# Kernel optimization log

Measured on AMD Instinct MI355X. Metric: run time of the kernel, lower is better.

Reference implementation:

```python
import jax, jax.numpy as jnp
import numpy as np

N_AUTHOR, N_FOS, N_INST, N_PAPER = 100000, 30000, 8000, 200000
D_IN, D_OUT = 128, 128
# (name, n_src, n_dst, n_edges)
RELS = [("aff", N_AUTHOR, N_INST, 150000), ("ita", N_INST, N_AUTHOR, 150000),
        ("writes", N_AUTHOR, N_PAPER, 500000), ("pta", N_PAPER, N_AUTHOR, 500000),
        ("cites", N_PAPER, N_PAPER, 1000000), ("topic", N_PAPER, N_FOS, 500000),
        ("ftp", N_FOS, N_PAPER, 500000)]
NODE_SIZES = {"author": N_AUTHOR, "fos": N_FOS, "inst": N_INST, "paper": N_PAPER}


def setup_inputs() -> dict:
    key = jax.random.key(0)
    ks = iter(jax.random.split(key, 64))
    inp = {}
    for nt, n in NODE_SIZES.items():
        inp[f"x_{nt}"] = jax.random.normal(next(ks), (n, D_IN), jnp.float32)
    for name, ns, nd, e in RELS:
        inp[f"src_{name}"] = jax.random.randint(next(ks), (e,), 0, ns, jnp.int64)
        inp[f"dst_{name}"] = jax.random.randint(next(ks), (e,), 0, nd, jnp.int64)
    w_scale = 1.0 / np.sqrt(D_IN)
    for nt in NODE_SIZES:
        inp[f"W_root_{nt}"] = jax.random.uniform(next(ks), (D_IN, D_OUT), jnp.float32, -w_scale, w_scale)
        inp[f"b_root_{nt}"] = jax.random.uniform(next(ks), (D_OUT,), jnp.float32, -w_scale, w_scale)
    for name, _, _, _ in RELS:
        inp[f"W_{name}"] = jax.random.uniform(next(ks), (D_IN, D_OUT), jnp.float32, -w_scale, w_scale)
    return inp


def _mean_agg(x_src, src, dst, n_dst):
    # gather source features along edges, mean-reduce into destinations
    msg = x_src[src]                                             # [E, D_IN]
    s = jax.ops.segment_sum(msg, dst, num_segments=n_dst)        # [n_dst, D_IN]
    cnt = jax.ops.segment_sum(jnp.ones_like(dst, dtype=x_src.dtype), dst, num_segments=n_dst)
    return s / jnp.maximum(cnt, 1.0)[:, None]                    # isolated nodes -> 0


def reference(x_author, x_fos, x_inst, x_paper,
              W_root_author, b_root_author, W_root_fos, b_root_fos,
              W_root_inst, b_root_inst, W_root_paper, b_root_paper,
              W_aff, W_ita, W_writes, W_pta, W_cites, W_topic, W_ftp,
              src_aff, dst_aff, src_ita, dst_ita, src_writes, dst_writes,
              src_pta, dst_pta, src_cites, dst_cites, src_topic, dst_topic,
              src_ftp, dst_ftp):
    # root (self) transforms
    out_author = x_author @ W_root_author + b_root_author
    out_fos = x_fos @ W_root_fos + b_root_fos
    out_inst = x_inst @ W_root_inst + b_root_inst
    out_paper = x_paper @ W_root_paper + b_root_paper
    # per-relation aggregate -> linear -> accumulate into destination type
    out_inst = out_inst + _mean_agg(x_author, src_aff, dst_aff, N_INST) @ W_aff
    out_author = out_author + _mean_agg(x_inst, src_ita, dst_ita, N_AUTHOR) @ W_ita
    out_paper = out_paper + _mean_agg(x_author, src_writes, dst_writes, N_PAPER) @ W_writes
    out_author = out_author + _mean_agg(x_paper, src_pta, dst_pta, N_AUTHOR) @ W_pta
    out_paper = out_paper + _mean_agg(x_paper, src_cites, dst_cites, N_PAPER) @ W_cites
    out_fos = out_fos + _mean_agg(x_paper, src_topic, dst_topic, N_FOS) @ W_topic
    out_paper = out_paper + _mean_agg(x_fos, src_ftp, dst_ftp, N_PAPER) @ W_ftp
    # concatenate per-type outputs (author, fos, inst, paper) along node axis
    return jnp.concatenate([out_author, out_fos, out_inst, out_paper], axis=0)
```

## Files before the change

### kernel.cpp

```cpp
#include <hip/hip_runtime.h>

#define N_AUTHOR 100000
#define N_FOS    30000
#define N_INST   8000
#define N_PAPER  200000
#define NCNT     838000
#define ETOT     3300000
#define NSHARD   (NCNT / 8)

#define NBA 1563
#define NBF 469
#define NBI 125
#define NBP 3125
#define NB_TOTAL (NBP + NBA + NBF + NBI)

#define B_AFF    0
#define B_ITA    8000
#define B_WRITES 108000
#define B_PTA    308000
#define B_CITES  408000
#define B_TOPIC  608000
#define B_FTP    638000

typedef __attribute__((ext_vector_type(8))) short short8v;
typedef __attribute__((ext_vector_type(4))) float float4v;
typedef unsigned short us;

__device__ __forceinline__ us f2bf(float f) {
  unsigned u = __float_as_uint(f);
  u = u + 0x7fffu + ((u >> 16) & 1u);
  return (us)(u >> 16);
}
#define BF2F(s) __uint_as_float(((unsigned)(us)(s)) << 16)

__device__ __forceinline__ void acc8(float4v& x, float4v& y, short8v h) {
  x[0] += BF2F(h[0]); x[1] += BF2F(h[1]); x[2] += BF2F(h[2]); x[3] += BF2F(h[3]);
  y[0] += BF2F(h[4]); y[1] += BF2F(h[5]); y[2] += BF2F(h[6]); y[3] += BF2F(h[7]);
}

__device__ __forceinline__ short8v pack8(float4v a, float4v b) {
  short8v h;
  h[0] = (short)f2bf(a[0]); h[1] = (short)f2bf(a[1]);
  h[2] = (short)f2bf(a[2]); h[3] = (short)f2bf(a[3]);
  h[4] = (short)f2bf(b[0]); h[5] = (short)f2bf(b[1]);
  h[6] = (short)f2bf(b[2]); h[7] = (short)f2bf(b[3]);
  return h;
}

#define O_CNT    0
#define O_OFFS   3352000
#define O_CURSOR 6704000
#define O_BTOT   10056000
#define O_CSR    10060096
#define O_WT     23260096
#define XB_AUTHOR 23620544
#define XB_FOS    49220544
#define XB_INST   56900544
#define XB_PAPER  58948544
#define WS_NEED_BF 110148544ULL

struct RelTab { const int* src; const int* dst; int E; int base; };
struct Rels { RelTab r[7]; };
struct WPtrs { const float* w[11]; };
struct XCvt { const float* x; us* xb; int n8; };

__global__ __launch_bounds__(256, 8) void prep(WPtrs P, us* __restrict__ wt,
                     int* __restrict__ cnt,
                     XCvt x0, XCvt x1, XCvt x2, XCvt x3,
                     Rels R, int doX) {
  int gsz = gridDim.x * blockDim.x;
  int gtid = blockIdx.x * blockDim.x + threadIdx.x;
  for (int i = gtid; i < 11 * 16384; i += gsz) {
    int mat = i >> 14, rem = i & 16383;
    int k = rem >> 7, n = rem & 127;
    wt[mat * 16384 + n * 128 + k] = f2bf(P.w[mat][rem]);
  }
  if (doX) {
    XCvt xc[4] = {x0, x1, x2, x3};
    #pragma unroll
    for (int a = 0; a < 4; ++a) {
      const float* xp = xc[a].x;
      short8v* xbp = (short8v*)xc[a].xb;
      int n8 = xc[a].n8;
      for (int i = gtid; i < n8; i += gsz) {
        float4v v0 = *(const float4v*)(xp + (size_t)i * 8);
        float4v v1 = *(const float4v*)(xp + (size_t)i * 8 + 4);
        xbp[i] = pack8(v0, v1);
      }
    }
  }
  const int cls = blockIdx.x & 7;
  const int lo = cls * NSHARD;
  const int hi = lo + NSHARD;
  const int sgsz = (gridDim.x >> 3) * 256;
  const int sgtid = (blockIdx.x >> 3) * 256 + threadIdx.x;
  #pragma unroll
  for (int rr = 0; rr < 7; ++rr) {
    const int* __restrict__ dst = R.r[rr].dst;
    const int E = R.r[rr].E, base = R.r[rr].base;
    for (int e = sgtid; e < E; e += sgsz) {
      int gd = base + dst[e];
      if (gd >= lo && gd < hi) atomicAdd(&cnt[gd], 1);
    }
  }
}

__global__ void scan1(const int* __restrict__ cnt, int* __restrict__ offs,
                      int* __restrict__ btot, int n) {
  __shared__ int sh[256];
  int tid = threadIdx.x;
  int base = blockIdx.x * 2048 + tid * 8;
  int v[8]; int s = 0;
  #pragma unroll
  for (int i = 0; i < 8; ++i) { v[i] = (base + i < n) ? cnt[base + i] : 0; s += v[i]; }
  sh[tid] = s; __syncthreads();
  for (int off = 1; off < 256; off <<= 1) {
    int t = (tid >= off) ? sh[tid - off] : 0;
    __syncthreads();
    sh[tid] += t;
    __syncthreads();
  }
  int excl = sh[tid] - s;
  if (tid == 255) btot[blockIdx.x] = sh[255];
  int run = excl;
  #pragma unroll
  for (int i = 0; i < 8; ++i) { if (base + i < n) offs[base + i] = run; run += v[i]; }
}

__global__ void scan23(int* __restrict__ offs, int* __restrict__ cursor,
                       const int* __restrict__ btot, int nb, int n) {
  __shared__ int sh[512];
  int tid = threadIdx.x;
  int v = (tid < nb) ? btot[tid] : 0;
  sh[tid] = v; __syncthreads();
  for (int off = 1; off < 512; off <<= 1) {
    int t = (tid >= off) ? sh[tid - off] : 0;
    __syncthreads();
    sh[tid] += t;
    __syncthreads();
  }
  int excl = sh[tid] - v;
  __syncthreads();
  sh[tid] = excl;
  __syncthreads();
  int gsz = gridDim.x * 512;
  for (int idx = blockIdx.x * 512 + tid; idx < n; idx += gsz) {
    int val = offs[idx] + sh[idx >> 11];
    offs[idx] = val;
    cursor[idx] = val;
  }
}

__global__ __launch_bounds__(256, 8) void fill_sh(Rels R, int* __restrict__ cursor,
                                                  int* __restrict__ csr) {
  const int cls = blockIdx.x & 7;
  const int lo = cls * NSHARD;
  const int hi = lo + NSHARD;
  const int gsz = (gridDim.x >> 3) * 256;
  const int gtid = (blockIdx.x >> 3) * 256 + threadIdx.x;
  #pragma unroll
  for (int rr = 0; rr < 7; ++rr) {
    const int* __restrict__ src = R.r[rr].src;
    const int* __restrict__ dst = R.r[rr].dst;
    const int E = R.r[rr].E, base = R.r[rr].base;
    for (int e = gtid; e < E; e += gsz) {
      int gd = base + dst[e];
      if (gd >= lo && gd < hi) {
        int p = atomicAdd(&cursor[gd], 1);
        csr[p] = src[e];
      }
    }
  }
}

template <int NSRC>
__device__ __forceinline__ void fused_body(
    const us* __restrict__ x0, const us* __restrict__ x1,
    const us* __restrict__ x2, const us* __restrict__ x3,
    const us* __restrict__ w0, const us* __restrict__ w1,
    const us* __restrict__ w2, const us* __restrict__ w3,
    int b1, int b2, int b3,
    const int* __restrict__ offs, const int* __restrict__ cnt,
    const int* __restrict__ csr,
    const float* __restrict__ bias, float* __restrict__ out, int n, int rb0) {
  const int lane = threadIdx.x & 63;
  const int wv = threadIdx.x >> 6;
  const int rb = rb0 + wv * 16;
  int ar = rb + (lane & 15); if (ar >= n) ar = n - 1;
  const int cw = (lane >> 4) * 8;

  const us* xs[4] = {x0, x1, x2, x3};
  const us* wsp[4] = {w0, w1, w2, w3};
  const int bases[4] = {0, b1, b2, b3};

  int stA[4], dgA[4];
  #pragma unroll
  for (int kb = 1; kb < NSRC; ++kb) {
    int gd = bases[kb] + ar;
    stA[kb] = offs[gd];
    dgA[kb] = cnt[gd];
  }

  float4v acc[8];
  #pragma unroll
  for (int i = 0; i < 8; ++i) acc[i] = (float4v)0.0f;

  #pragma unroll
  for (int kb = 0; kb < NSRC; ++kb) {
    short8v af[4];
    if (kb == 0) {
      const us* rp = xs[0] + (size_t)ar * 128 + cw;
      #pragma unroll
      for (int ks = 0; ks < 4; ++ks)
        af[ks] = *(const short8v*)(rp + ks * 32);
    } else {
      const int st = stA[kb], deg = dgA[kb];
      const us* xb = xs[kb];
      float4v a0[4], a1[4];
      #pragma unroll
      for (int ks = 0; ks < 4; ++ks) { a0[ks] = (float4v)0.f; a1[ks] = (float4v)0.f; }
      int j = 0;
      int s0 = 0, s1 = 0;
      if (deg >= 2) { s0 = csr[st]; s1 = csr[st + 1]; }
      for (; j + 2 <= deg; j += 2) {
        const us* p0 = xb + (size_t)s0 * 128 + cw;
        const us* p1 = xb + (size_t)s1 * 128 + cw;
        if (j + 4 <= deg) { s0 = csr[st + j + 2]; s1 = csr[st + j + 3]; }
        #pragma unroll
        for (int ks = 0; ks < 4; ++ks) {
          short8v h0 = *(const short8v*)(p0 + ks * 32);
          short8v h1 = *(const short8v*)(p1 + ks * 32);
          acc8(a0[ks], a1[ks], h0);
          acc8(a0[ks], a1[ks], h1);
        }
      }
      if (j < deg) {
        int sl = csr[st + j];
        const us* p0 = xb + (size_t)sl * 128 + cw;
        #pragma unroll
        for (int ks = 0; ks < 4; ++ks) {
          short8v h0 = *(const short8v*)(p0 + ks * 32);
          acc8(a0[ks], a1[ks], h0);
        }
      }
      float sc = 1.0f / (float)((deg > 0) ? deg : 1);
      #pragma unroll
      for (int ks = 0; ks < 4; ++ks)
        af[ks] = pack8(a0[ks] * sc, a1[ks] * sc);
    }
    const us* wb = wsp[kb] + (size_t)(lane & 15) * 128 + cw;
    #pragma unroll
    for (int ct = 0; ct < 8; ++ct) {
      short8v bfr[4];
      #pragma unroll
      for (int ks = 0; ks < 4; ++ks)
        bfr[ks] = *(const short8v*)(wb + ct * 2048 + ks * 32);
      #pragma unroll
      for (int ks = 0; ks < 4; ++ks)
        acc[ct] = __builtin_amdgcn_mfma_f32_16x16x32_bf16(af[ks], bfr[ks], acc[ct], 0, 0, 0);
    }
  }
  #pragma unroll
  for (int ct = 0; ct < 8; ++ct) {
    #pragma unroll
    for (int i = 0; i < 4; ++i) {
      int g = rb + (lane >> 4) * 4 + i;
      if (g < n) {
        int col = ct * 16 + (lane & 15);
        out[(size_t)g * 128 + col] = acc[ct][i] + bias[col];
      }
    }
  }
}

__global__ __launch_bounds__(256, 6) void fused_all(
    const us* __restrict__ xbA, const us* __restrict__ xbF,
    const us* __restrict__ xbI, const us* __restrict__ xbP,
    const us* __restrict__ wt,
    const int* __restrict__ offs, const int* __restrict__ cnt,
    const int* __restrict__ csr,
    const float* __restrict__ bA, const float* __restrict__ bF,
    const float* __restrict__ bI, const float* __restrict__ bP,
    float* __restrict__ out) {
  const int bid = blockIdx.x;
  if (bid < NBP) {
    fused_body<4>(xbP, xbA, xbP, xbF,
                  wt + 3 * 16384, wt + 6 * 16384, wt + 8 * 16384, wt + 10 * 16384,
                  B_WRITES, B_CITES, B_FTP, offs, cnt, csr,
                  bP, out + (size_t)138000 * 128, N_PAPER, bid * 64);
  } else if (bid < NBP + NBA) {
    fused_body<3>(xbA, xbI, xbP, nullptr,
                  wt + 0 * 16384, wt + 5 * 16384, wt + 7 * 16384, nullptr,
                  B_ITA, B_PTA, 0, offs, cnt, csr,
                  bA, out, N_AUTHOR, (bid - NBP) * 64);
  } else if (bid < NBP + NBA + NBF) {
    fused_body<2>(xbF, xbP, nullptr, nullptr,
                  wt + 1 * 16384, wt + 9 * 16384, nullptr, nullptr,
                  B_TOPIC, 0, 0, offs, cnt, csr,
                  bF, out + (size_t)100000 * 128, N_FOS, (bid - NBP - NBA) * 64);
  } else {
    fused_body<2>(xbI, xbA, nullptr, nullptr,
                  wt + 2 * 16384, wt + 4 * 16384, nullptr, nullptr,
                  B_AFF, 0, 0, offs, cnt, csr,
                  bI, out + (size_t)130000 * 128, N_INST, (bid - NBP - NBA - NBF) * 64);
  }
}

typedef float4v f4;
__global__ __launch_bounds__(256, 4) void fb_gemm(
    const float* __restrict__ x0, const float* __restrict__ x1,
    const float* __restrict__ x2, const float* __restrict__ x3,
    const us* __restrict__ w0, const us* __restrict__ w1,
    const us* __restrict__ w2, const us* __restrict__ w3,
    int nsrc, int b1, int b2, int b3,
    const int* __restrict__ offs, const int* __restrict__ cnt,
    const int* __restrict__ csr,
    const float* __restrict__ bias, float* __restrict__ out, int n) {
  const int lane = threadIdx.x & 63;
  const int wv = threadIdx.x >> 6;
  const int rb = blockIdx.x * 64 + wv * 16;
  int ar = rb + (lane & 15); if (ar >= n) ar = n - 1;
  const int cw = (lane >> 4) * 8;
  const float* xs[4] = {x0, x1, x2, x3};
  const us* wsp[4] = {w0, w1, w2, w3};
  const int bases[4] = {0, b1, b2, b3};
  float4v acc[8];
  #pragma unroll
  for (int i = 0; i < 8; ++i) acc[i] = (float4v)0.0f;
  for (int kb = 0; kb < nsrc; ++kb) {
    short8v af[4];
    const float* xb = xs[kb];
    if (kb == 0) {
      const float* rp = xb + (size_t)ar * 128 + cw;
      #pragma unroll
      for (int ks = 0; ks < 4; ++ks) {
        f4 u = *(const f4*)(rp + ks * 32);
        f4 v = *(const f4*)(rp + ks * 32 + 4);
        af[ks] = pack8(u, v);
      }
    } else {
      int gd = bases[kb] + ar;
      int st = offs[gd];
      int deg = cnt[gd];
      f4 a0[4], a1[4];
      #pragma unroll
      for (int ks = 0; ks < 4; ++ks) { a0[ks] = (f4)0.f; a1[ks] = (f4)0.f; }
      for (int j = 0; j < deg; ++j) {
        int s0 = csr[st + j];
        const float* p0 = xb + (size_t)s0 * 128 + cw;
        #pragma unroll
        for (int ks = 0; ks < 4; ++ks) {
          a0[ks] += *(const f4*)(p0 + ks * 32);
          a1[ks] += *(const f4*)(p0 + ks * 32 + 4);
        }
      }
      float sc = 1.0f / (float)((deg > 0) ? deg : 1);
      #pragma unroll
      for (int ks = 0; ks < 4; ++ks)
        af[ks] = pack8(a0[ks] * sc, a1[ks] * sc);
    }
    const us* wb = wsp[kb] + (size_t)(lane & 15) * 128 + cw;
    #pragma unroll
    for (int ct = 0; ct < 8; ++ct) {
      short8v bfr[4];
      #pragma unroll
      for (int ks = 0; ks < 4; ++ks)
        bfr[ks] = *(const short8v*)(wb + ct * 2048 + ks * 32);
      #pragma unroll
      for (int ks = 0; ks < 4; ++ks)
        acc[ct] = __builtin_amdgcn_mfma_f32_16x16x32_bf16(af[ks], bfr[ks], acc[ct], 0, 0, 0);
    }
  }
  #pragma unroll
  for (int ct = 0; ct < 8; ++ct) {
    #pragma unroll
    for (int i = 0; i < 4; ++i) {
      int g = rb + (lane >> 4) * 4 + i;
      if (g < n) {
        int col = ct * 16 + (lane & 15);
        out[(size_t)g * 128 + col] = acc[ct][i] + bias[col];
      }
    }
  }
}

extern "C" void kernel_launch(void* const* d_in, const int* in_sizes, int n_in,
                              void* d_out, int out_size, void* d_ws, size_t ws_size,
                              hipStream_t stream) {
  const float* x_author = (const float*)d_in[0];
  const float* x_fos    = (const float*)d_in[1];
  const float* x_inst   = (const float*)d_in[2];
  const float* x_paper  = (const float*)d_in[3];

  Rels R;
  const int E[7]  = {150000, 150000, 500000, 500000, 1000000, 500000, 500000};
  const int ND[7] = {N_INST, N_AUTHOR, N_PAPER, N_AUTHOR, N_PAPER, N_FOS, N_PAPER};
  int base = 0;
  for (int r = 0; r < 7; ++r) {
    R.r[r].src = (const int*)d_in[4 + 2 * r];
    R.r[r].dst = (const int*)d_in[5 + 2 * r];
    R.r[r].E = E[r];
    R.r[r].base = base;
    base += ND[r];
  }

  char* ws = (char*)d_ws;
  int* cnt    = (int*)(ws + O_CNT);
  int* offs   = (int*)(ws + O_OFFS);
  int* cursor = (int*)(ws + O_CURSOR);
  int* btot   = (int*)(ws + O_BTOT);
  int* csr    = (int*)(ws + O_CSR);
  us* wt  = (us*)(ws + O_WT);
  us* xbA = (us*)(ws + XB_AUTHOR);
  us* xbF = (us*)(ws + XB_FOS);
  us* xbI = (us*)(ws + XB_INST);
  us* xbP = (us*)(ws + XB_PAPER);

  const int useBF = (ws_size >= WS_NEED_BF) ? 1 : 0;

  WPtrs WP;
  WP.w[0] = (const float*)d_in[18];
  WP.w[1] = (const float*)d_in[20];
  WP.w[2] = (const float*)d_in[22];
  WP.w[3] = (const float*)d_in[24];
  for (int r = 0; r < 7; ++r) WP.w[4 + r] = (const float*)d_in[26 + r];

  XCvt xcA = {x_author, xbA, N_AUTHOR * 16};
  XCvt xcF = {x_fos,    xbF, N_FOS * 16};
  XCvt xcI = {x_inst,   xbI, N_INST * 16};
  XCvt xcP = {x_paper,  xbP, N_PAPER * 16};

  hipMemsetAsync(cnt, 0, (size_t)NCNT * 4, stream);
  prep<<<2048, 256, 0, stream>>>(WP, wt, cnt, xcA, xcF, xcI, xcP, R, useBF);
  scan1<<<410, 256, 0, stream>>>(cnt, offs, btot, NCNT);
  scan23<<<1024, 512, 0, stream>>>(offs, cursor, btot, 410, NCNT);
  fill_sh<<<2048, 256, 0, stream>>>(R, cursor, csr);

  float* out = (float*)d_out;
  const float* bA = (const float*)d_in[19];
  const float* bF = (const float*)d_in[21];
  const float* bI = (const float*)d_in[23];
  const float* bP = (const float*)d_in[25];

  if (useBF) {
    fused_all<<<NB_TOTAL, 256, 0, stream>>>(xbA, xbF, xbI, xbP, wt,
                                            offs, cnt, csr,
                                            bA, bF, bI, bP, out);
  } else {
    fb_gemm<<<NBA, 256, 0, stream>>>(
        x_author, x_inst, x_paper, nullptr,
        wt + 0 * 16384, wt + 5 * 16384, wt + 7 * 16384, nullptr,
        3, B_ITA, B_PTA, 0, offs, cnt, csr, bA, out, N_AUTHOR);
    fb_gemm<<<NBF, 256, 0, stream>>>(
        x_fos, x_paper, nullptr, nullptr,
        wt + 1 * 16384, wt + 9 * 16384, nullptr, nullptr,
        2, B_TOPIC, 0, 0, offs, cnt, csr, bF, out + (size_t)100000 * 128, N_FOS);
    fb_gemm<<<NBI, 256, 0, stream>>>(
        x_inst, x_author, nullptr, nullptr,
        wt + 2 * 16384, wt + 4 * 16384, nullptr, nullptr,
        2, B_AFF, 0, 0, offs, cnt, csr, bI, out + (size_t)130000 * 128, N_INST);
    fb_gemm<<<NBP, 256, 0, stream>>>(
        x_paper, x_author, x_paper, x_fos,
        wt + 3 * 16384, wt + 6 * 16384, wt + 8 * 16384, wt + 10 * 16384,
        4, B_WRITES, B_CITES, B_FTP, offs, cnt, csr, bP,
        out + (size_t)138000 * 128, N_PAPER);
  }
}
```

Before: 817.9 us.

## Sort destination rows by total degree to balance wavefront gather work

Adds a counting sort (histogram, scan, scatter) that orders the destination rows of each node type by their combined in-degree, capped at 63. The fused gather+MFMA kernel then processes rows in that order, so the 16 rows sharing a wavefront have similar neighbor counts and lanes diverge less in the gather loops. This costs three extra small kernels, one indirection per row, scattered output stores, and the removal of the explicit csr index prefetch.

```diff
diff --git a/kernel.cpp b/kernel.cpp
--- a/kernel.cpp
+++ b/kernel.cpp
@@ -7,6 +7,8 @@
 #define NCNT     838000
 #define ETOT     3300000
 #define NSHARD   (NCNT / 8)
+#define NROWS    338000
+#define NBLK_S   661
 
 #define NBA 1563
 #define NBF 469
@@ -21,6 +23,11 @@
 #define B_CITES  408000
 #define B_TOPIC  608000
 #define B_FTP    638000
+
+#define OB_A 0
+#define OB_F 100000
+#define OB_I 130000
+#define OB_P 138000
 
 typedef __attribute__((ext_vector_type(8))) short short8v;
 typedef __attribute__((ext_vector_type(4))) float float4v;
@@ -57,7 +64,11 @@
 #define XB_FOS    49220544
 #define XB_INST   56900544
 #define XB_PAPER  58948544
-#define WS_NEED_BF 110148544ULL
+#define O_ORDER  110148544
+#define O_KEYB   111500544
+#define O_BH     111838560
+#define O_BB     112515424
+#define WS_NEED_BF 113192288ULL
 
 struct RelTab { const int* src; const int* dst; int E; int base; };
 struct Rels { RelTab r[7]; };
@@ -101,6 +112,76 @@
     for (int e = sgtid; e < E; e += sgsz) {
       int gd = base + dst[e];
       if (gd >= lo && gd < hi) atomicAdd(&cnt[gd], 1);
+    }
+  }
+}
+
+__global__ __launch_bounds__(256) void ks_hist(const int* __restrict__ cnt,
+                                               unsigned char* __restrict__ keyb,
+                                               int* __restrict__ bh) {
+  __shared__ int lh[256];
+  lh[threadIdx.x] = 0;
+  __syncthreads();
+  #pragma unroll
+  for (int r = 0; r < 2; ++r) {
+    int u = blockIdx.x * 512 + r * 256 + threadIdx.x;
+    if (u < NROWS) {
+      int t, loc, key;
+      if (u < 100000)      { t = 0; loc = u;          key = cnt[B_ITA + loc] + cnt[B_PTA + loc]; }
+      else if (u < 130000) { t = 1; loc = u - 100000; key = cnt[B_TOPIC + loc]; }
+      else if (u < 138000) { t = 2; loc = u - 130000; key = cnt[B_AFF + loc]; }
+      else                 { t = 3; loc = u - 138000; key = cnt[B_WRITES + loc] + cnt[B_CITES + loc] + cnt[B_FTP + loc]; }
+      int k = (key > 63) ? 63 : key;
+      int bin = t * 64 + k;
+      keyb[u] = (unsigned char)bin;
+      atomicAdd(&lh[bin], 1);
+    }
+  }
+  __syncthreads();
+  bh[blockIdx.x * 256 + threadIdx.x] = lh[threadIdx.x];
+}
+
+__global__ void hscan(const int* __restrict__ bh, int* __restrict__ bb, int nblk) {
+  __shared__ int sh[256];
+  const int b = threadIdx.x;
+  int s = 0;
+  int B = 0;
+  for (; B + 8 <= nblk; B += 8) {
+    int v[8];
+    #pragma unroll
+    for (int q = 0; q < 8; ++q) v[q] = bh[(B + q) * 256 + b];
+    #pragma unroll
+    for (int q = 0; q < 8; ++q) { bb[(B + q) * 256 + b] = s; s += v[q]; }
+  }
+  for (; B < nblk; ++B) { int v = bh[B * 256 + b]; bb[B * 256 + b] = s; s += v; }
+  int tot = s;
+  sh[b] = s;
+  __syncthreads();
+  for (int off = 1; off < 256; off <<= 1) {
+    int t = (b >= off) ? sh[b - off] : 0;
+    __syncthreads();
+    sh[b] += t;
+    __syncthreads();
+  }
+  int excl = sh[b] - tot;
+  for (B = 0; B < nblk; ++B) bb[B * 256 + b] += excl;
+}
+
+__global__ __launch_bounds__(256) void ks_scat(const unsigned char* __restrict__ keyb,
+                                               const int* __restrict__ bb,
+                                               int* __restrict__ order) {
+  __shared__ int lc[256];
+  lc[threadIdx.x] = 0;
+  __syncthreads();
+  #pragma unroll
+  for (int r = 0; r < 2; ++r) {
+    int u = blockIdx.x * 512 + r * 256 + threadIdx.x;
+    if (u < NROWS) {
+      int bin = keyb[u];
+      int off = atomicAdd(&lc[bin], 1);
+      int loc = (u < 100000) ? u : (u < 130000) ? u - 100000
+              : (u < 138000) ? u - 130000 : u - 138000;
+      order[bb[blockIdx.x * 256 + bin] + off] = loc;
     }
   }
 }
@@ -181,26 +262,19 @@
     const us* __restrict__ w2, const us* __restrict__ w3,
     int b1, int b2, int b3,
     const int* __restrict__ offs, const int* __restrict__ cnt,
-    const int* __restrict__ csr,
+    const int* __restrict__ csr, const int* __restrict__ order, int obase,
     const float* __restrict__ bias, float* __restrict__ out, int n, int rb0) {
   const int lane = threadIdx.x & 63;
   const int wv = threadIdx.x >> 6;
   const int rb = rb0 + wv * 16;
-  int ar = rb + (lane & 15); if (ar >= n) ar = n - 1;
+  int slot = rb + (lane & 15); if (slot >= n) slot = n - 1;
+  const int g = order[obase + slot];
   const int cw = (lane >> 4) * 8;
 
   const us* xs[4] = {x0, x1, x2, x3};
   const us* wsp[4] = {w0, w1, w2, w3};
   const int bases[4] = {0, b1, b2, b3};
 
-  int stA[4], dgA[4];
-  #pragma unroll
-  for (int kb = 1; kb < NSRC; ++kb) {
-    int gd = bases[kb] + ar;
-    stA[kb] = offs[gd];
-    dgA[kb] = cnt[gd];
-  }
-
   float4v acc[8];
   #pragma unroll
   for (int i = 0; i < 8; ++i) acc[i] = (float4v)0.0f;
@@ -209,23 +283,23 @@
   for (int kb = 0; kb < NSRC; ++kb) {
     short8v af[4];
     if (kb == 0) {
-      const us* rp = xs[0] + (size_t)ar * 128 + cw;
+      const us* rp = xs[0] + (size_t)g * 128 + cw;
       #pragma unroll
       for (int ks = 0; ks < 4; ++ks)
         af[ks] = *(const short8v*)(rp + ks * 32);
     } else {
-      const int st = stA[kb], deg = dgA[kb];
+      int gd = bases[kb] + g;
+      int st = offs[gd];
+      int deg = cnt[gd];
       const us* xb = xs[kb];
       float4v a0[4], a1[4];
       #pragma unroll
       for (int ks = 0; ks < 4; ++ks) { a0[ks] = (float4v)0.f; a1[ks] = (float4v)0.f; }
       int j = 0;
-      int s0 = 0, s1 = 0;
-      if (deg >= 2) { s0 = csr[st]; s1 = csr[st + 1]; }
       for (; j + 2 <= deg; j += 2) {
+        int s0 = csr[st + j], s1 = csr[st + j + 1];
         const us* p0 = xb + (size_t)s0 * 128 + cw;
         const us* p1 = xb + (size_t)s1 * 128 + cw;
-        if (j + 4 <= deg) { s0 = csr[st + j + 2]; s1 = csr[st + j + 3]; }
         #pragma unroll
         for (int ks = 0; ks < 4; ++ks) {
           short8v h0 = *(const short8v*)(p0 + ks * 32);
@@ -235,8 +309,8 @@
         }
       }
       if (j < deg) {
-        int sl = csr[st + j];
-        const us* p0 = xb + (size_t)sl * 128 + cw;
+        int s0 = csr[st + j];
+        const us* p0 = xb + (size_t)s0 * 128 + cw;
         #pragma unroll
         for (int ks = 0; ks < 4; ++ks) {
           short8v h0 = *(const short8v*)(p0 + ks * 32);
@@ -260,14 +334,19 @@
         acc[ct] = __builtin_amdgcn_mfma_f32_16x16x32_bf16(af[ks], bfr[ks], acc[ct], 0, 0, 0);
     }
   }
+  int grow[4];
+  #pragma unroll
+  for (int i = 0; i < 4; ++i) {
+    int srow = rb + (lane >> 4) * 4 + i;
+    grow[i] = (srow < n) ? order[obase + srow] : -1;
+  }
   #pragma unroll
   for (int ct = 0; ct < 8; ++ct) {
     #pragma unroll
     for (int i = 0; i < 4; ++i) {
-      int g = rb + (lane >> 4) * 4 + i;
-      if (g < n) {
+      if (grow[i] >= 0) {
         int col = ct * 16 + (lane & 15);
-        out[(size_t)g * 128 + col] = acc[ct][i] + bias[col];
+        out[(size_t)grow[i] * 128 + col] = acc[ct][i] + bias[col];
       }
     }
   }
@@ -278,7 +357,7 @@
     const us* __restrict__ xbI, const us* __restrict__ xbP,
     const us* __restrict__ wt,
     const int* __restrict__ offs, const int* __restrict__ cnt,
-    const int* __restrict__ csr,
+    const int* __restrict__ csr, const int* __restrict__ order,
     const float* __restrict__ bA, const float* __restrict__ bF,
     const float* __restrict__ bI, const float* __restrict__ bP,
     float* __restrict__ out) {
@@ -286,22 +365,22 @@
   if (bid < NBP) {
     fused_body<4>(xbP, xbA, xbP, xbF,
                   wt + 3 * 16384, wt + 6 * 16384, wt + 8 * 16384, wt + 10 * 16384,
-                  B_WRITES, B_CITES, B_FTP, offs, cnt, csr,
+                  B_WRITES, B_CITES, B_FTP, offs, cnt, csr, order, OB_P,
                   bP, out + (size_t)138000 * 128, N_PAPER, bid * 64);
   } else if (bid < NBP + NBA) {
     fused_body<3>(xbA, xbI, xbP, nullptr,
                   wt + 0 * 16384, wt + 5 * 16384, wt + 7 * 16384, nullptr,
-                  B_ITA, B_PTA, 0, offs, cnt, csr,
+                  B_ITA, B_PTA, 0, offs, cnt, csr, order, OB_A,
                   bA, out, N_AUTHOR, (bid - NBP) * 64);
   } else if (bid < NBP + NBA + NBF) {
     fused_body<2>(xbF, xbP, nullptr, nullptr,
                   wt + 1 * 16384, wt + 9 * 16384, nullptr, nullptr,
-                  B_TOPIC, 0, 0, offs, cnt, csr,
+                  B_TOPIC, 0, 0, offs, cnt, csr, order, OB_F,
                   bF, out + (size_t)100000 * 128, N_FOS, (bid - NBP - NBA) * 64);
   } else {
     fused_body<2>(xbI, xbA, nullptr, nullptr,
                   wt + 2 * 16384, wt + 4 * 16384, nullptr, nullptr,
-                  B_AFF, 0, 0, offs, cnt, csr,
+                  B_AFF, 0, 0, offs, cnt, csr, order, OB_I,
                   bI, out + (size_t)130000 * 128, N_INST, (bid - NBP - NBA - NBF) * 64);
   }
 }
@@ -415,6 +494,10 @@
   us* xbF = (us*)(ws + XB_FOS);
   us* xbI = (us*)(ws + XB_INST);
   us* xbP = (us*)(ws + XB_PAPER);
+  int* order = (int*)(ws + O_ORDER);
+  unsigned char* keyb = (unsigned char*)(ws + O_KEYB);
+  int* bh = (int*)(ws + O_BH);
+  int* bb = (int*)(ws + O_BB);
 
   const int useBF = (ws_size >= WS_NEED_BF) ? 1 : 0;
 
@@ -432,9 +515,6 @@
 
   hipMemsetAsync(cnt, 0, (size_t)NCNT * 4, stream);
   prep<<<2048, 256, 0, stream>>>(WP, wt, cnt, xcA, xcF, xcI, xcP, R, useBF);
-  scan1<<<410, 256, 0, stream>>>(cnt, offs, btot, NCNT);
-  scan23<<<1024, 512, 0, stream>>>(offs, cursor, btot, 410, NCNT);
-  fill_sh<<<2048, 256, 0, stream>>>(R, cursor, csr);
 
   float* out = (float*)d_out;
   const float* bA = (const float*)d_in[19];
@@ -443,10 +523,22 @@
   const float* bP = (const float*)d_in[25];
 
   if (useBF) {
+    ks_hist<<<NBLK_S, 256, 0, stream>>>(cnt, keyb, bh);
+    hscan<<<1, 256, 0, stream>>>(bh, bb, NBLK_S);
+    ks_scat<<<NBLK_S, 256, 0, stream>>>(keyb, bb, order);
+
+    scan1<<<410, 256, 0, stream>>>(cnt, offs, btot, NCNT);
+    scan23<<<1024, 512, 0, stream>>>(offs, cursor, btot, 410, NCNT);
+    fill_sh<<<2048, 256, 0, stream>>>(R, cursor, csr);
+
     fused_all<<<NB_TOTAL, 256, 0, stream>>>(xbA, xbF, xbI, xbP, wt,
-                                            offs, cnt, csr,
+                                            offs, cnt, csr, order,
                                             bA, bF, bI, bP, out);
   } else {
+    scan1<<<410, 256, 0, stream>>>(cnt, offs, btot, NCNT);
+    scan23<<<1024, 512, 0, stream>>>(offs, cursor, btot, 410, NCNT);
+    fill_sh<<<2048, 256, 0, stream>>>(R, cursor, csr);
+
     fb_gemm<<<NBA, 256, 0, stream>>>(
         x_author, x_inst, x_paper, nullptr,
         wt + 0 * 16384, wt + 5 * 16384, wt + 7 * 16384, nullptr,
```

Result: slower. 986.9 us (+20.7%).
